# Performance work log

Hardware: AMD Instinct MI355X
Metric: run time of the kernel (lower is better)

The kernel has to match this reference:

```python
import jax, jax.numpy as jnp
import numpy as np

D = 512      # model dim
H = 8        # heads
HD = D // H  # head dim = 64
NQ = 2048    # n_query
NC = 4096    # n_context
EPS = 1e-5   # LayerNorm eps (torch default)


def setup_inputs() -> dict:
    key = jax.random.key(0)
    ks = jax.random.split(key, 12)
    s = 0.02
    return {
        "query_repr": jax.random.normal(ks[0], (NQ, D), dtype=jnp.float32),
        "context_repr": jax.random.normal(ks[1], (NC, D), dtype=jnp.float32),
        "query_coords": jax.random.uniform(ks[2], (NQ, 2), dtype=jnp.float32) * 10.0,
        "context_coords": jax.random.uniform(ks[3], (NC, 2), dtype=jnp.float32) * 10.0,
        "Wq": jax.random.normal(ks[4], (D, D), dtype=jnp.float32) * s,
        "bq": jnp.zeros((D,), jnp.float32),
        "Wk": jax.random.normal(ks[5], (D, D), dtype=jnp.float32) * s,
        "bk": jnp.zeros((D,), jnp.float32),
        "Wv": jax.random.normal(ks[6], (D, D), dtype=jnp.float32) * s,
        "bv": jnp.zeros((D,), jnp.float32),
        "Wo": jax.random.normal(ks[7], (D, D), dtype=jnp.float32) * s,
        "bo": jnp.zeros((D,), jnp.float32),
        "ln_g": jnp.ones((D,), jnp.float32),
        "ln_b": jnp.zeros((D,), jnp.float32),
        "log_scale": jnp.array(0.0, jnp.float32),          # log_distance_scale
        "bias_per_head": jnp.ones((H,), jnp.float32),      # distance_bias_per_head
    }


def reference(query_repr, context_repr, query_coords, context_coords,
              Wq, bq, Wk, bk, Wv, bv, Wo, bo, ln_g, ln_b,
              log_scale, bias_per_head):
    # pairwise Euclidean distances (NQ, NC)
    diff = query_coords[:, None, :] - context_coords[None, :, :]
    dist = jnp.sqrt(jnp.sum(diff * diff, axis=-1))
    # per-head additive attention bias (H, NQ, NC)
    bias = (-jnp.exp(log_scale) * dist)[None, :, :] * bias_per_head[:, None, None]

    # multi-head attention (batch=1, eval mode so dropout is identity)
    q = (query_repr @ Wq.T + bq).reshape(NQ, H, HD).transpose(1, 0, 2)    # (H, NQ, HD)
    k = (context_repr @ Wk.T + bk).reshape(NC, H, HD).transpose(1, 0, 2)  # (H, NC, HD)
    v = (context_repr @ Wv.T + bv).reshape(NC, H, HD).transpose(1, 0, 2)  # (H, NC, HD)

    scale = 1.0 / jnp.sqrt(jnp.float32(HD))
    scores = jnp.einsum('hqd,hkd->hqk', q, k) * scale + bias              # (H, NQ, NC)
    attn = jax.nn.softmax(scores, axis=-1)
    ctx = jnp.einsum('hqk,hkd->hqd', attn, v)                             # (H, NQ, HD)
    attended = ctx.transpose(1, 0, 2).reshape(NQ, D) @ Wo.T + bo          # (NQ, D)

    # residual + LayerNorm
    x = attended + query_repr
    mu = jnp.mean(x, axis=-1, keepdims=True)
    var = jnp.mean((x - mu) ** 2, axis=-1, keepdims=True)
    return (x - mu) / jnp.sqrt(var + EPS) * ln_g + ln_b
```

## Files before the change

kernel.cpp:

```cpp
#include <hip/hip_runtime.h>

#define D 512
#define H 8
#define HD 64
#define NQ 2048
#define NC 4096
#define SPLIT 8
#define CLEN (NC / SPLIT)
#define NT (CLEN / 32)
#define M0 3.0f
#define KP2 136
#define VP 40

typedef __attribute__((ext_vector_type(8))) short short8;
typedef __attribute__((ext_vector_type(4))) short short4v;
typedef __attribute__((ext_vector_type(4))) float float4v;
typedef __attribute__((ext_vector_type(4))) int int4v;

__device__ inline float bf2f(short s) {
    unsigned int u = ((unsigned int)(unsigned short)s) << 16;
    return __builtin_bit_cast(float, u);
}
__device__ inline short f2bf(float f) {
    unsigned int u = __builtin_bit_cast(unsigned int, f);
    u = (u + 0x7FFF + ((u >> 16) & 1)) >> 16;
    return (short)u;
}
__device__ inline int cvtpk(float a, float b) {
    int w;
    asm("v_cvt_pk_bf16_f32 %0, %1, %2" : "=v"(w) : "v"(a), "v"(b));
    return w;
}

__global__ __launch_bounds__(256) void cast_all(
    const float* __restrict__ s0, const float* __restrict__ s1,
    const float* __restrict__ s2, const float* __restrict__ s3,
    const float* __restrict__ s4, const float* __restrict__ s5,
    short* __restrict__ dst)
{
    int i = blockIdx.x * 256 + threadIdx.x;
    const float* src; int off;
    if      (i < 262144) { src = s0; off = i; }
    else if (i < 786432) { src = s1; off = i - 262144; }
    else if (i < 851968) { src = s2; off = i - 786432; }
    else if (i < 917504) { src = s3; off = i - 851968; }
    else if (i < 983040) { src = s4; off = i - 917504; }
    else                 { src = s5; off = i - 983040; }
    float4v v = ((const float4v*)src)[off];
    short4v o;
    o.x = f2bf(v.x); o.y = f2bf(v.y); o.z = f2bf(v.z); o.w = f2bf(v.w);
    ((short4v*)dst)[i] = o;
}

__global__ __launch_bounds__(256) void gemm_bt_bias(
    const short* __restrict__ X, const short* __restrict__ W,
    const float* __restrict__ bias, short* __restrict__ out, int M)
{
    int wave = threadIdx.x >> 6, lane = threadIdx.x & 63;
    int gt = blockIdx.x * 4 + wave;
    int tm = gt >> 3;
    int tg = gt & 7;
    if (tm >= (M >> 4)) return;
    int l15 = lane & 15, quad = lane >> 4;
    const short* xp = X + (tm * 16 + l15) * D + quad * 8;
    const short* wp = W + (tg * 64 + l15) * D + quad * 8;
    float4v a0 = {0,0,0,0}, a1 = {0,0,0,0}, a2 = {0,0,0,0}, a3 = {0,0,0,0};
#pragma unroll
    for (int k = 0; k < D; k += 32) {
        short8 a  = *(const short8*)(xp + k);
        short8 b0 = *(const short8*)(wp + k);
        short8 b1 = *(const short8*)(wp + 16 * D + k);
        short8 b2 = *(const short8*)(wp + 32 * D + k);
        short8 b3 = *(const short8*)(wp + 48 * D + k);
        a0 = __builtin_amdgcn_mfma_f32_16x16x32_bf16(a, b0, a0, 0, 0, 0);
        a1 = __builtin_amdgcn_mfma_f32_16x16x32_bf16(a, b1, a1, 0, 0, 0);
        a2 = __builtin_amdgcn_mfma_f32_16x16x32_bf16(a, b2, a2, 0, 0, 0);
        a3 = __builtin_amdgcn_mfma_f32_16x16x32_bf16(a, b3, a3, 0, 0, 0);
    }
    int orow = tm * 16 + quad * 4;
    float4v accs[4] = {a0, a1, a2, a3};
#pragma unroll
    for (int j = 0; j < 4; j++) {
        int col = tg * 64 + j * 16 + l15;
        float bv = bias[col];
#pragma unroll
        for (int r = 0; r < 4; r++)
            out[(orow + r) * D + col] = f2bf(accs[j][r] + bv);
    }
}

__global__ __launch_bounds__(256) void gemm_qkv(
    const short* __restrict__ Xq, const short* __restrict__ Xc,
    const short* __restrict__ Wq, const short* __restrict__ Wk,
    const short* __restrict__ Wv,
    const float* __restrict__ bq, const float* __restrict__ bk,
    const float* __restrict__ bv,
    short* __restrict__ Qout, short* __restrict__ Kout,
    short* __restrict__ VoutT)
{
    int wave = threadIdx.x >> 6, lane = threadIdx.x & 63;
    int l15 = lane & 15, quad = lane >> 4;
    int blk = blockIdx.x;
    if (blk < 256) {
        int gt = blk * 4 + wave;
        int tm = gt >> 3, tg = gt & 7;
        const short* xp = Xq + (tm * 16 + l15) * D + quad * 8;
        const short* wp = Wq + (tg * 64 + l15) * D + quad * 8;
        float4v a0 = {0,0,0,0}, a1 = {0,0,0,0}, a2 = {0,0,0,0}, a3 = {0,0,0,0};
#pragma unroll
        for (int k = 0; k < D; k += 32) {
            short8 a  = *(const short8*)(xp + k);
            short8 b0 = *(const short8*)(wp + k);
            short8 b1 = *(const short8*)(wp + 16 * D + k);
            short8 b2 = *(const short8*)(wp + 32 * D + k);
            short8 b3 = *(const short8*)(wp + 48 * D + k);
            a0 = __builtin_amdgcn_mfma_f32_16x16x32_bf16(a, b0, a0, 0, 0, 0);
            a1 = __builtin_amdgcn_mfma_f32_16x16x32_bf16(a, b1, a1, 0, 0, 0);
            a2 = __builtin_amdgcn_mfma_f32_16x16x32_bf16(a, b2, a2, 0, 0, 0);
            a3 = __builtin_amdgcn_mfma_f32_16x16x32_bf16(a, b3, a3, 0, 0, 0);
        }
        int orow = tm * 16 + quad * 4;
        float4v accs[4] = {a0, a1, a2, a3};
#pragma unroll
        for (int j = 0; j < 4; j++) {
            int col = tg * 64 + j * 16 + l15;
            float bb = bq[col];
#pragma unroll
            for (int r = 0; r < 4; r++)
                Qout[(orow + r) * D + col] = f2bf(accs[j][r] + bb);
        }
    } else {
        int gt = (blk - 256) * 4 + wave;
        int tm = gt >> 3, tg = gt & 7;
        const short* xp  = Xc + (tm * 16 + l15) * D + quad * 8;
        const short* wkp = Wk + (tg * 64 + l15) * D + quad * 8;
        const short* wvp = Wv + (tg * 64 + l15) * D + quad * 8;
        float4v k0 = {0,0,0,0}, k1 = {0,0,0,0}, k2 = {0,0,0,0}, k3 = {0,0,0,0};
        float4v v0 = {0,0,0,0}, v1 = {0,0,0,0}, v2 = {0,0,0,0}, v3 = {0,0,0,0};
#pragma unroll
        for (int k = 0; k < D; k += 32) {
            short8 a   = *(const short8*)(xp + k);
            short8 bk0 = *(const short8*)(wkp + k);
            short8 bk1 = *(const short8*)(wkp + 16 * D + k);
            short8 bk2 = *(const short8*)(wkp + 32 * D + k);
            short8 bk3 = *(const short8*)(wkp + 48 * D + k);
            short8 bv0 = *(const short8*)(wvp + k);
            short8 bv1 = *(const short8*)(wvp + 16 * D + k);
            short8 bv2 = *(const short8*)(wvp + 32 * D + k);
            short8 bv3 = *(const short8*)(wvp + 48 * D + k);
            k0 = __builtin_amdgcn_mfma_f32_16x16x32_bf16(a, bk0, k0, 0, 0, 0);
            k1 = __builtin_amdgcn_mfma_f32_16x16x32_bf16(a, bk1, k1, 0, 0, 0);
            k2 = __builtin_amdgcn_mfma_f32_16x16x32_bf16(a, bk2, k2, 0, 0, 0);
            k3 = __builtin_amdgcn_mfma_f32_16x16x32_bf16(a, bk3, k3, 0, 0, 0);
            v0 = __builtin_amdgcn_mfma_f32_16x16x32_bf16(a, bv0, v0, 0, 0, 0);
            v1 = __builtin_amdgcn_mfma_f32_16x16x32_bf16(a, bv1, v1, 0, 0, 0);
            v2 = __builtin_amdgcn_mfma_f32_16x16x32_bf16(a, bv2, v2, 0, 0, 0);
            v3 = __builtin_amdgcn_mfma_f32_16x16x32_bf16(a, bv3, v3, 0, 0, 0);
        }
        int orow = tm * 16 + quad * 4;
        {
            float4v accs[4] = {k0, k1, k2, k3};
#pragma unroll
            for (int j = 0; j < 4; j++) {
                int col = tg * 64 + j * 16 + l15;
                float bb = bk[col];
#pragma unroll
                for (int r = 0; r < 4; r++)
                    Kout[(orow + r) * D + col] = f2bf(accs[j][r] + bb);
            }
        }
        {
            int a = (orow & 31) >> 2;
            int posb = (a < 4) ? (8 * a) : (8 * (a - 4) + 4);
            int cp = (orow & ~31) + posb;
            float4v accs[4] = {v0, v1, v2, v3};
#pragma unroll
            for (int j = 0; j < 4; j++) {
                int col = tg * 64 + j * 16 + l15;
                float bb = bv[col];
                short4v o;
#pragma unroll
                for (int r = 0; r < 4; r++) o[r] = f2bf(accs[j][r] + bb);
                *(short4v*)(VoutT + (size_t)col * NC + cp) = o;
            }
        }
    }
}

__global__ __launch_bounds__(256) void gemm_res_ln(
    const short* __restrict__ X, const short* __restrict__ W,
    const float* __restrict__ bias, const float* __restrict__ resid,
    const float* __restrict__ g, const float* __restrict__ b,
    float* __restrict__ out)
{
    __shared__ float redS[4][4][4];
    __shared__ float redV[4][4][4];

    int wave = threadIdx.x >> 6, lane = threadIdx.x & 63;
    int l15 = lane & 15, quad = lane >> 4;
    int tm = blockIdx.x;
    const short* xp  = X + (tm * 16 + l15) * D + quad * 8;
    const short* wp0 = W + ((2 * wave) * 64 + l15) * D + quad * 8;
    const short* wp1 = wp0 + 64 * D;
    float4v a00 = {0,0,0,0}, a01 = {0,0,0,0}, a02 = {0,0,0,0}, a03 = {0,0,0,0};
    float4v a10 = {0,0,0,0}, a11 = {0,0,0,0}, a12 = {0,0,0,0}, a13 = {0,0,0,0};
#pragma unroll
    for (int k = 0; k < D; k += 32) {
        short8 a   = *(const short8*)(xp + k);
        short8 b00 = *(const short8*)(wp0 + k);
        short8 b01 = *(const short8*)(wp0 + 16 * D + k);
        short8 b02 = *(const short8*)(wp0 + 32 * D + k);
        short8 b03 = *(const short8*)(wp0 + 48 * D + k);
        short8 b10 = *(const short8*)(wp1 + k);
        short8 b11 = *(const short8*)(wp1 + 16 * D + k);
        short8 b12 = *(const short8*)(wp1 + 32 * D + k);
        short8 b13 = *(const short8*)(wp1 + 48 * D + k);
        a00 = __builtin_amdgcn_mfma_f32_16x16x32_bf16(a, b00, a00, 0, 0, 0);
        a01 = __builtin_amdgcn_mfma_f32_16x16x32_bf16(a, b01, a01, 0, 0, 0);
        a02 = __builtin_amdgcn_mfma_f32_16x16x32_bf16(a, b02, a02, 0, 0, 0);
        a03 = __builtin_amdgcn_mfma_f32_16x16x32_bf16(a, b03, a03, 0, 0, 0);
        a10 = __builtin_amdgcn_mfma_f32_16x16x32_bf16(a, b10, a10, 0, 0, 0);
        a11 = __builtin_amdgcn_mfma_f32_16x16x32_bf16(a, b11, a11, 0, 0, 0);
        a12 = __builtin_amdgcn_mfma_f32_16x16x32_bf16(a, b12, a12, 0, 0, 0);
        a13 = __builtin_amdgcn_mfma_f32_16x16x32_bf16(a, b13, a13, 0, 0, 0);
    }
    int orow = tm * 16 + quad * 4;
    float v[2][4][4];
    float4v accs[2][4] = {{a00, a01, a02, a03}, {a10, a11, a12, a13}};
#pragma unroll
    for (int t = 0; t < 2; t++) {
#pragma unroll
        for (int j = 0; j < 4; j++) {
            int col = (2 * wave + t) * 64 + j * 16 + l15;
            float bv = bias[col];
#pragma unroll
            for (int r = 0; r < 4; r++)
                v[t][j][r] = accs[t][j][r] + bv + resid[(orow + r) * D + col];
        }
    }
    float ps[4];
#pragma unroll
    for (int r = 0; r < 4; r++) {
        float s = 0.f;
#pragma unroll
        for (int t = 0; t < 2; t++)
#pragma unroll
            for (int j = 0; j < 4; j++) s += v[t][j][r];
#pragma unroll
        for (int off = 1; off < 16; off <<= 1) s += __shfl_xor(s, off);
        ps[r] = s;
    }
    if (l15 == 0) {
#pragma unroll
        for (int r = 0; r < 4; r++) redS[wave][quad][r] = ps[r];
    }
    __syncthreads();
    float mu[4];
#pragma unroll
    for (int r = 0; r < 4; r++)
        mu[r] = (redS[0][quad][r] + redS[1][quad][r] +
                 redS[2][quad][r] + redS[3][quad][r]) * (1.f / D);
#pragma unroll
    for (int r = 0; r < 4; r++) {
        float s = 0.f;
#pragma unroll
        for (int t = 0; t < 2; t++)
#pragma unroll
            for (int j = 0; j < 4; j++) {
                float d = v[t][j][r] - mu[r];
                s += d * d;
            }
#pragma unroll
        for (int off = 1; off < 16; off <<= 1) s += __shfl_xor(s, off);
        ps[r] = s;
    }
    if (l15 == 0) {
#pragma unroll
        for (int r = 0; r < 4; r++) redV[wave][quad][r] = ps[r];
    }
    __syncthreads();
    float rstd[4];
#pragma unroll
    for (int r = 0; r < 4; r++) {
        float var = (redV[0][quad][r] + redV[1][quad][r] +
                     redV[2][quad][r] + redV[3][quad][r]) * (1.f / D);
        rstd[r] = rsqrtf(var + 1e-5f);
    }
#pragma unroll
    for (int t = 0; t < 2; t++) {
#pragma unroll
        for (int j = 0; j < 4; j++) {
            int col = (2 * wave + t) * 64 + j * 16 + l15;
            float gc = g[col], bc = b[col];
#pragma unroll
            for (int r = 0; r < 4; r++)
                out[(orow + r) * D + col] =
                    (v[t][j][r] - mu[r]) * rstd[r] * gc + bc;
        }
    }
}

__global__ __launch_bounds__(256) void gemm_bt_bias_res_f32(
    const short* __restrict__ X, const short* __restrict__ W,
    const float* __restrict__ bias, const float* __restrict__ resid,
    float* __restrict__ out, int M)
{
    int wave = threadIdx.x >> 6, lane = threadIdx.x & 63;
    int gt = blockIdx.x * 4 + wave;
    int tm = gt >> 3;
    int tg = gt & 7;
    if (tm >= (M >> 4)) return;
    int l15 = lane & 15, quad = lane >> 4;
    const short* xp = X + (tm * 16 + l15) * D + quad * 8;
    const short* wp = W + (tg * 64 + l15) * D + quad * 8;
    float4v a0 = {0,0,0,0}, a1 = {0,0,0,0}, a2 = {0,0,0,0}, a3 = {0,0,0,0};
#pragma unroll
    for (int k = 0; k < D; k += 32) {
        short8 a  = *(const short8*)(xp + k);
        short8 b0 = *(const short8*)(wp + k);
        short8 b1 = *(const short8*)(wp + 16 * D + k);
        short8 b2 = *(const short8*)(wp + 32 * D + k);
        short8 b3 = *(const short8*)(wp + 48 * D + k);
        a0 = __builtin_amdgcn_mfma_f32_16x16x32_bf16(a, b0, a0, 0, 0, 0);
        a1 = __builtin_amdgcn_mfma_f32_16x16x32_bf16(a, b1, a1, 0, 0, 0);
        a2 = __builtin_amdgcn_mfma_f32_16x16x32_bf16(a, b2, a2, 0, 0, 0);
        a3 = __builtin_amdgcn_mfma_f32_16x16x32_bf16(a, b3, a3, 0, 0, 0);
    }
    int orow = tm * 16 + quad * 4;
    float4v accs[4] = {a0, a1, a2, a3};
#pragma unroll
    for (int j = 0; j < 4; j++) {
        int col = tg * 64 + j * 16 + l15;
        float bv = bias[col];
#pragma unroll
        for (int r = 0; r < 4; r++) {
            int q = orow + r;
            out[q * D + col] = accs[j][r] + bv + resid[q * D + col];
        }
    }
}

__global__ __launch_bounds__(256) void attn_mfma_split9(
    const short* __restrict__ Q, const short* __restrict__ K,
    const short* __restrict__ Vp,
    const float* __restrict__ qc, const float* __restrict__ cc,
    const float* __restrict__ log_scale, const float* __restrict__ bph,
    short* __restrict__ Opart, float* __restrict__ Lpart)
{
    __shared__ __align__(16) short Klds[2][32 * KP2];
    __shared__ __align__(16) short Vlds[2][128 * VP];
    __shared__ __align__(16) float ccl[512];

    int tid = threadIdx.x;
    int wave = tid >> 6, lane = tid & 63;
    int h0 = blockIdx.y * 2;
    int sp = blockIdx.z;
    int q0 = blockIdx.x * 64 + wave * 16;
    int quad = lane >> 4, l15 = lane & 15;
    int cbase = sp * CLEN;

    const float LOG2E = 1.4426950408889634f;
    const float escale = 0.125f * LOG2E;
    const float M0L = M0 * LOG2E;
    float ebase = __expf(log_scale[0]);
    float bh0 = ebase * bph[h0] * LOG2E;
    float bh1 = ebase * bph[h0 + 1] * LOG2E;

    const short* qp = Q + (q0 + l15) * D + h0 * HD + quad * 8;
    short8 qa0_0 = *(const short8*)(qp);
    short8 qa1_0 = *(const short8*)(qp + 32);
    short8 qa0_1 = *(const short8*)(qp + 64);
    short8 qa1_1 = *(const short8*)(qp + 96);

    float qx = qc[(q0 + l15) * 2];
    float qy = qc[(q0 + l15) * 2 + 1];

    float lacc0 = 0.f, lacc1 = 0.f;
    float4v O00 = {0,0,0,0}, O01 = {0,0,0,0}, O02 = {0,0,0,0}, O03 = {0,0,0,0};
    float4v O10 = {0,0,0,0}, O11 = {0,0,0,0}, O12 = {0,0,0,0}, O13 = {0,0,0,0};

    int kr_ = tid >> 3, kc_ = tid & 7;
    int vr_ = tid >> 2, vc_ = tid & 3;
    const short* kg  = K + (size_t)h0 * HD + kc_ * 8;
    const short* vg0 = Vp + (size_t)(h0 * HD + vr_) * NC + vc_ * 8;
    const short* vg1 = Vp + (size_t)(h0 * HD + 64 + vr_) * NC + vc_ * 8;
    short* kw0a = &Klds[0][kr_ * KP2 + kc_ * 8];
    short* kw1a = &Klds[1][kr_ * KP2 + kc_ * 8];
    short* vw0a = &Vlds[0][vr_ * VP + vc_ * 8];
    short* vw0b = &Vlds[0][(64 + vr_) * VP + vc_ * 8];
    short* vw1a = &Vlds[1][vr_ * VP + vc_ * 8];
    short* vw1b = &Vlds[1][(64 + vr_) * VP + vc_ * 8];

    short8 rka, rkb, rva, rvb;

#define LOADR(c0_)                                                             \
    {                                                                          \
        const short* kp_ = kg + (size_t)((c0_) + kr_) * D;                     \
        rka = *(const short8*)(kp_);                                           \
        rkb = *(const short8*)(kp_ + 64);                                      \
        rva = *(const short8*)(vg0 + (c0_));                                   \
        rvb = *(const short8*)(vg1 + (c0_));                                   \
    }

#define DSW0 { *(short8*)kw0a = rka; *(short8*)(kw0a + 64) = rkb;              \
               *(short8*)vw0a = rva; *(short8*)vw0b = rvb; }
#define DSW1 { *(short8*)kw1a = rka; *(short8*)(kw1a + 64) = rkb;              \
               *(short8*)vw1a = rva; *(short8*)vw1b = rvb; }

    const float2* ccp = (const float2*)ccl;

#define HEAD(hoff, QA0, QA1, BH, LACC, OA, OB, OC, OD)                         \
    {                                                                          \
        short8 k00 = *(const short8*)(kb + l15 * KP2 + (hoff) + quad * 8);     \
        short8 k01 = *(const short8*)(kb + l15 * KP2 + (hoff) + 32 + quad * 8);\
        short8 k10 = *(const short8*)(kb + (16 + l15) * KP2 + (hoff) + quad * 8);\
        short8 k11 = *(const short8*)(kb + (16 + l15) * KP2 + (hoff) + 32 + quad * 8);\
        float4v s0 = {0,0,0,0}, s1 = {0,0,0,0};                                \
        s0 = __builtin_amdgcn_mfma_f32_16x16x32_bf16(k00, QA0, s0, 0, 0, 0);   \
        s0 = __builtin_amdgcn_mfma_f32_16x16x32_bf16(k01, QA1, s0, 0, 0, 0);   \
        s1 = __builtin_amdgcn_mfma_f32_16x16x32_bf16(k10, QA0, s1, 0, 0, 0);   \
        s1 = __builtin_amdgcn_mfma_f32_16x16x32_bf16(k11, QA1, s1, 0, 0, 0);   \
        short8 v0 = *(const short8*)(vb + ((hoff) / 64 * 64 + l15) * VP + quad * 8);       \
        short8 v1 = *(const short8*)(vb + ((hoff) / 64 * 64 + 16 + l15) * VP + quad * 8);  \
        short8 v2 = *(const short8*)(vb + ((hoff) / 64 * 64 + 32 + l15) * VP + quad * 8);  \
        short8 v3 = *(const short8*)(vb + ((hoff) / 64 * 64 + 48 + l15) * VP + quad * 8);  \
        float p00 = exp2f(__fmaf_rn(s0[0], escale, __fmaf_rn(-(BH), dA0, -M0L)));\
        float p01 = exp2f(__fmaf_rn(s0[1], escale, __fmaf_rn(-(BH), dA1, -M0L)));\
        float p02 = exp2f(__fmaf_rn(s0[2], escale, __fmaf_rn(-(BH), dA2, -M0L)));\
        float p03 = exp2f(__fmaf_rn(s0[3], escale, __fmaf_rn(-(BH), dA3, -M0L)));\
        float p10 = exp2f(__fmaf_rn(s1[0], escale, __fmaf_rn(-(BH), dB0, -M0L)));\
        float p11 = exp2f(__fmaf_rn(s1[1], escale, __fmaf_rn(-(BH), dB1, -M0L)));\
        float p12 = exp2f(__fmaf_rn(s1[2], escale, __fmaf_rn(-(BH), dB2, -M0L)));\
        float p13 = exp2f(__fmaf_rn(s1[3], escale, __fmaf_rn(-(BH), dB3, -M0L)));\
        LACC += ((p00 + p01) + (p02 + p03)) + ((p10 + p11) + (p12 + p13));     \
        int4v pw;                                                              \
        pw.x = cvtpk(p00, p01); pw.y = cvtpk(p02, p03);                        \
        pw.z = cvtpk(p10, p11); pw.w = cvtpk(p12, p13);                        \
        short8 pa = __builtin_bit_cast(short8, pw);                            \
        OA = __builtin_amdgcn_mfma_f32_16x16x32_bf16(pa, v0, OA, 0, 0, 0);     \
        OB = __builtin_amdgcn_mfma_f32_16x16x32_bf16(pa, v1, OB, 0, 0, 0);     \
        OC = __builtin_amdgcn_mfma_f32_16x16x32_bf16(pa, v2, OC, 0, 0, 0);     \
        OD = __builtin_amdgcn_mfma_f32_16x16x32_bf16(pa, v3, OD, 0, 0, 0);     \
    }

#define COMPUTE_TILE(B, lo)                                                    \
    {                                                                          \
        const short* kb = &Klds[B][0];                                         \
        const short* vb = &Vlds[B][0];                                         \
        float2 ca0 = ccp[(lo) + 4 * quad + 0], cb0 = ccp[(lo) + 16 + 4 * quad + 0];\
        float2 ca1 = ccp[(lo) + 4 * quad + 1], cb1 = ccp[(lo) + 16 + 4 * quad + 1];\
        float2 ca2 = ccp[(lo) + 4 * quad + 2], cb2 = ccp[(lo) + 16 + 4 * quad + 2];\
        float2 ca3 = ccp[(lo) + 4 * quad + 3], cb3 = ccp[(lo) + 16 + 4 * quad + 3];\
        float dx, dy;                                                          \
        dx = qx - ca0.x; dy = qy - ca0.y;                                      \
        float dA0 = __builtin_amdgcn_sqrtf(__fmaf_rn(dx, dx, dy * dy));        \
        dx = qx - ca1.x; dy = qy - ca1.y;                                      \
        float dA1 = __builtin_amdgcn_sqrtf(__fmaf_rn(dx, dx, dy * dy));        \
        dx = qx - ca2.x; dy = qy - ca2.y;                                      \
        float dA2 = __builtin_amdgcn_sqrtf(__fmaf_rn(dx, dx, dy * dy));        \
        dx = qx - ca3.x; dy = qy - ca3.y;                                      \
        float dA3 = __builtin_amdgcn_sqrtf(__fmaf_rn(dx, dx, dy * dy));        \
        dx = qx - cb0.x; dy = qy - cb0.y;                                      \
        float dB0 = __builtin_amdgcn_sqrtf(__fmaf_rn(dx, dx, dy * dy));        \
        dx = qx - cb1.x; dy = qy - cb1.y;                                      \
        float dB1 = __builtin_amdgcn_sqrtf(__fmaf_rn(dx, dx, dy * dy));        \
        dx = qx - cb2.x; dy = qy - cb2.y;                                      \
        float dB2 = __builtin_amdgcn_sqrtf(__fmaf_rn(dx, dx, dy * dy));        \
        dx = qx - cb3.x; dy = qy - cb3.y;                                      \
        float dB3 = __builtin_amdgcn_sqrtf(__fmaf_rn(dx, dx, dy * dy));        \
        HEAD(0,  qa0_0, qa1_0, bh0, lacc0, O00, O01, O02, O03)                 \
        HEAD(64, qa0_1, qa1_1, bh1, lacc1, O10, O11, O12, O13)                 \
    }

    ((float2*)ccl)[tid] = ((const float2*)cc)[cbase + tid];
    LOADR(cbase);
    DSW0;
    LOADR(cbase + 32);
    __syncthreads();

    for (int t = 0; t < NT - 2; t += 2) {
        int c0 = cbase + t * 32;
        if (t == 8) {
            ((float2*)ccl)[tid] = ((const float2*)cc)[cbase + 256 + tid];
            __syncthreads();
        }
        DSW1;
        LOADR(c0 + 64);
        COMPUTE_TILE(0, (t & 7) * 32);
        __syncthreads();
        DSW0;
        LOADR(c0 + 96);
        COMPUTE_TILE(1, (t & 7) * 32 + 32);
        __syncthreads();
    }
    DSW1;
    COMPUTE_TILE(0, 192);
    __syncthreads();
    COMPUTE_TILE(1, 224);

#undef LOADR
#undef DSW0
#undef DSW1
#undef HEAD
#undef COMPUTE_TILE

    lacc0 += __shfl_xor(lacc0, 16);
    lacc0 += __shfl_xor(lacc0, 32);
    lacc1 += __shfl_xor(lacc1, 16);
    lacc1 += __shfl_xor(lacc1, 32);

    long base0 = (long)(sp * H + h0) * NQ;
    long base1 = base0 + NQ;
    float4v Oarr0[4] = {O00, O01, O02, O03};
    float4v Oarr1[4] = {O10, O11, O12, O13};
#pragma unroll
    for (int t = 0; t < 4; t++) {
#pragma unroll
        for (int r = 0; r < 4; r++) {
            int q = q0 + quad * 4 + r;
            Opart[(base0 + q) * HD + t * 16 + l15] = f2bf(Oarr0[t][r]);
            Opart[(base1 + q) * HD + t * 16 + l15] = f2bf(Oarr1[t][r]);
        }
    }
    if (lane < 16) {
        Lpart[base0 + q0 + lane] = lacc0;
        Lpart[base1 + q0 + lane] = lacc1;
    }
}

__global__ __launch_bounds__(256) void attn_combine(
    const short* __restrict__ Opart, const float* __restrict__ Lpart,
    short* __restrict__ Att)
{
    int id = blockIdx.x * 256 + threadIdx.x;
    int d = id & 63;
    int q = (id >> 6) & (NQ - 1);
    int h = id >> 17;
    float L = 0.f, acc = 0.f;
#pragma unroll
    for (int s = 0; s < SPLIT; s++) {
        long b = (long)(s * H + h) * NQ + q;
        L   += Lpart[b];
        acc += bf2f(Opart[b * HD + d]);
    }
    Att[q * D + h * HD + d] = f2bf(acc / L);
}

__global__ __launch_bounds__(256) void attn_mfma(
    const short* __restrict__ Q, const short* __restrict__ K,
    const short* __restrict__ V,
    const float* __restrict__ qc, const float* __restrict__ cc,
    const float* __restrict__ log_scale, const float* __restrict__ bph,
    short* __restrict__ out)
{
    __shared__ short Vt[HD][48];
    __shared__ short P[4][16][48];
    int wave = threadIdx.x >> 6, lane = threadIdx.x & 63;
    int h = blockIdx.y;
    int q0 = blockIdx.x * 64 + wave * 16;
    int quad = lane >> 4, l15 = lane & 15;
    const float scale = 0.125f;
    float bh = __expf(log_scale[0]) * bph[h];
    const short* qp = Q + (q0 + l15) * D + h * HD + quad * 8;
    short8 qa0 = *(const short8*)(qp);
    short8 qa1 = *(const short8*)(qp + 32);
    float qx[4], qy[4];
#pragma unroll
    for (int r = 0; r < 4; r++) {
        int q = q0 + quad * 4 + r;
        qx[r] = qc[q * 2]; qy[r] = qc[q * 2 + 1];
    }
    float m[4], l[4];
    float4v O[4];
#pragma unroll
    for (int r = 0; r < 4; r++) { m[r] = -1e30f; l[r] = 0.f; }
#pragma unroll
    for (int t = 0; t < 4; t++) O[t] = (float4v){0.f, 0.f, 0.f, 0.f};
    for (int c0 = 0; c0 < NC; c0 += 32) {
        __syncthreads();
        {
            int c = threadIdx.x >> 3;
            int dblk = (threadIdx.x & 7) * 8;
            short8 vv = *(const short8*)(V + (c0 + c) * D + h * HD + dblk);
#pragma unroll
            for (int j = 0; j < 8; j++) Vt[dblk + j][c] = vv[j];
        }
        const short* kp0 = K + (c0 + l15) * D + h * HD + quad * 8;
        const short* kp1 = kp0 + 16 * D;
        short8 kb00 = *(const short8*)(kp0);
        short8 kb01 = *(const short8*)(kp0 + 32);
        short8 kb10 = *(const short8*)(kp1);
        short8 kb11 = *(const short8*)(kp1 + 32);
        float4v s0 = {0,0,0,0}, s1 = {0,0,0,0};
        s0 = __builtin_amdgcn_mfma_f32_16x16x32_bf16(qa0, kb00, s0, 0, 0, 0);
        s0 = __builtin_amdgcn_mfma_f32_16x16x32_bf16(qa1, kb01, s0, 0, 0, 0);
        s1 = __builtin_amdgcn_mfma_f32_16x16x32_bf16(qa0, kb10, s1, 0, 0, 0);
        s1 = __builtin_amdgcn_mfma_f32_16x16x32_bf16(qa1, kb11, s1, 0, 0, 0);
        int cA = c0 + l15, cB = cA + 16;
        float cxA = cc[cA * 2], cyA = cc[cA * 2 + 1];
        float cxB = cc[cB * 2], cyB = cc[cB * 2 + 1];
#pragma unroll
        for (int r = 0; r < 4; r++) {
            float dxA = qx[r] - cxA, dyA = qy[r] - cyA;
            float dxB = qx[r] - cxB, dyB = qy[r] - cyB;
            float v0 = s0[r] * scale - bh * sqrtf(dxA * dxA + dyA * dyA);
            float v1 = s1[r] * scale - bh * sqrtf(dxB * dxB + dyB * dyB);
            float mx = fmaxf(v0, v1);
#pragma unroll
            for (int off = 1; off < 16; off <<= 1) mx = fmaxf(mx, __shfl_xor(mx, off));
            float mnew = fmaxf(m[r], mx);
            float alpha = __expf(m[r] - mnew);
            float p0 = __expf(v0 - mnew);
            float p1 = __expf(v1 - mnew);
            float ps = p0 + p1;
#pragma unroll
            for (int off = 1; off < 16; off <<= 1) ps += __shfl_xor(ps, off);
            l[r] = l[r] * alpha + ps;
            m[r] = mnew;
#pragma unroll
            for (int t = 0; t < 4; t++) O[t][r] *= alpha;
            P[wave][quad * 4 + r][l15]      = f2bf(p0);
            P[wave][quad * 4 + r][16 + l15] = f2bf(p1);
        }
        __syncthreads();
        short8 pa = *(const short8*)(&P[wave][l15][quad * 8]);
#pragma unroll
        for (int t = 0; t < 4; t++) {
            short8 vb = *(const short8*)(&Vt[t * 16 + l15][quad * 8]);
            O[t] = __builtin_amdgcn_mfma_f32_16x16x32_bf16(pa, vb, O[t], 0, 0, 0);
        }
    }
#pragma unroll
    for (int t = 0; t < 4; t++) {
#pragma unroll
        for (int r = 0; r < 4; r++) {
            int q = q0 + quad * 4 + r;
            out[q * D + h * HD + t * 16 + l15] = f2bf(O[t][r] / l[r]);
        }
    }
}

__global__ __launch_bounds__(256) void layernorm_kernel(
    const float* __restrict__ X, const float* __restrict__ g,
    const float* __restrict__ b, float* __restrict__ out)
{
    int wave = threadIdx.x >> 6, lane = threadIdx.x & 63;
    int row = blockIdx.x * 4 + wave;
    const float* xp = X + row * D;
    float v[8];
    float s = 0.f;
#pragma unroll
    for (int i = 0; i < 8; i++) { v[i] = xp[lane + i * 64]; s += v[i]; }
#pragma unroll
    for (int off = 1; off < 64; off <<= 1) s += __shfl_xor(s, off);
    float mu = s * (1.f / D);
    float var = 0.f;
#pragma unroll
    for (int i = 0; i < 8; i++) { float d = v[i] - mu; var += d * d; }
#pragma unroll
    for (int off = 1; off < 64; off <<= 1) var += __shfl_xor(var, off);
    float rstd = rsqrtf(var * (1.f / D) + 1e-5f);
#pragma unroll
    for (int i = 0; i < 8; i++) {
        int c = lane + i * 64;
        out[row * D + c] = (v[i] - mu) * rstd * g[c] + b[c];
    }
}

extern "C" void kernel_launch(void* const* d_in, const int* in_sizes, int n_in,
                              void* d_out, int out_size, void* d_ws, size_t ws_size,
                              hipStream_t stream) {
    const float* query_repr     = (const float*)d_in[0];
    const float* context_repr   = (const float*)d_in[1];
    const float* query_coords   = (const float*)d_in[2];
    const float* context_coords = (const float*)d_in[3];
    const float* Wq = (const float*)d_in[4];
    const float* bq = (const float*)d_in[5];
    const float* Wk = (const float*)d_in[6];
    const float* bk = (const float*)d_in[7];
    const float* Wv = (const float*)d_in[8];
    const float* bv = (const float*)d_in[9];
    const float* Wo = (const float*)d_in[10];
    const float* bo = (const float*)d_in[11];
    const float* ln_g = (const float*)d_in[12];
    const float* ln_b = (const float*)d_in[13];
    const float* log_scale = (const float*)d_in[14];
    const float* bph = (const float*)d_in[15];

    short* ws = (short*)d_ws;
    short* Xq_bf = ws;
    short* Xc_bf = Xq_bf + NQ * D;
    short* Wq_bf = Xc_bf + NC * D;
    short* Wk_bf = Wq_bf + D * D;
    short* Wv_bf = Wk_bf + D * D;
    short* Wo_bf = Wv_bf + D * D;
    short* Qw  = Wo_bf + D * D;
    short* Kw  = Qw + NQ * D;
    short* Vw  = Kw + NC * D;
    short* Att = Vw + NC * D;
    float* Xf  = (float*)(Att + NQ * D);
    short* Opart = (short*)(Xf + NQ * D);
    float* Lpart = (float*)(Opart + (size_t)SPLIT * H * NQ * HD);
    size_t ws_needed_split = ((char*)(Lpart + (size_t)SPLIT * H * NQ)) - (char*)d_ws;

    cast_all<<<dim3(4096), 256, 0, stream>>>(
        query_repr, context_repr, Wq, Wk, Wv, Wo, Xq_bf);

    if (ws_size >= ws_needed_split) {
        gemm_qkv<<<dim3(768), 256, 0, stream>>>(
            Xq_bf, Xc_bf, Wq_bf, Wk_bf, Wv_bf, bq, bk, bv, Qw, Kw, Vw);
        attn_mfma_split9<<<dim3(NQ / 64, H / 2, SPLIT), 256, 0, stream>>>(
            Qw, Kw, Vw, query_coords, context_coords, log_scale, bph,
            Opart, Lpart);
        attn_combine<<<dim3(H * NQ * HD / 256), 256, 0, stream>>>(
            Opart, Lpart, Att);
        gemm_res_ln<<<dim3(NQ / 16), 256, 0, stream>>>(
            Att, Wo_bf, bo, query_repr, ln_g, ln_b, (float*)d_out);
    } else {
        gemm_bt_bias<<<dim3((NQ / 16) * 8 / 4), 256, 0, stream>>>(
            Xq_bf, Wq_bf, bq, Qw, NQ);
        gemm_bt_bias<<<dim3((NC / 16) * 8 / 4), 256, 0, stream>>>(
            Xc_bf, Wk_bf, bk, Kw, NC);
        gemm_bt_bias<<<dim3((NC / 16) * 8 / 4), 256, 0, stream>>>(
            Xc_bf, Wv_bf, bv, Vw, NC);
        attn_mfma<<<dim3(NQ / 64, H), 256, 0, stream>>>(
            Qw, Kw, Vw, query_coords, context_coords, log_scale, bph, Att);
        gemm_bt_bias_res_f32<<<dim3((NQ / 16) * 8 / 4), 256, 0, stream>>>(
            Att, Wo_bf, bo, query_repr, Xf, NQ);
        layernorm_kernel<<<dim3(NQ / 4), 256, 0, stream>>>(
            Xf, ln_g, ln_b, (float*)d_out);
    }
}
```

Baseline: 202.6 us.

## Rewrite QKV projection as LDS-tiled double-buffered MFMA GEMM

Replaces the per-wave QKV projection, which streamed A and B fragments straight from global memory, with a block-tiled GEMM. Each block computes a 128x64 tile with 32-wide K slices staged through padded, double-buffered shared memory, and the next slice's global load overlaps the current MFMAs. This increases operand reuse and cuts redundant global and L2 traffic. In exchange it gives up the shared A load that K and V used to get from one fused pass, and adds barriers and LDS traffic.

```diff
diff --git a/kernel.cpp b/kernel.cpp
--- a/kernel.cpp
+++ b/kernel.cpp
@@ -11,6 +11,11 @@
 #define M0 3.0f
 #define KP2 136
 #define VP 40
+
+#define TBM 128
+#define TBN 64
+#define TBK 32
+#define TPAD 40
 
 typedef __attribute__((ext_vector_type(8))) short short8;
 typedef __attribute__((ext_vector_type(4))) short short4v;
@@ -89,7 +94,7 @@
     }
 }
 
-__global__ __launch_bounds__(256) void gemm_qkv(
+__global__ __launch_bounds__(256) void gemm_qkv_tiled(
     const short* __restrict__ Xq, const short* __restrict__ Xc,
     const short* __restrict__ Wq, const short* __restrict__ Wk,
     const short* __restrict__ Wv,
@@ -98,90 +103,128 @@
     short* __restrict__ Qout, short* __restrict__ Kout,
     short* __restrict__ VoutT)
 {
-    int wave = threadIdx.x >> 6, lane = threadIdx.x & 63;
-    int l15 = lane & 15, quad = lane >> 4;
+    __shared__ __align__(16) short Ab[2][TBM * TPAD];
+    __shared__ __align__(16) short Bb[2][TBN * TPAD];
+
+    int tid = threadIdx.x;
+    int wave = tid >> 6, lane = tid & 63;
+    int quad = lane >> 4, l15 = lane & 15;
+
     int blk = blockIdx.x;
-    if (blk < 256) {
-        int gt = blk * 4 + wave;
-        int tm = gt >> 3, tg = gt & 7;
-        const short* xp = Xq + (tm * 16 + l15) * D + quad * 8;
-        const short* wp = Wq + (tg * 64 + l15) * D + quad * 8;
-        float4v a0 = {0,0,0,0}, a1 = {0,0,0,0}, a2 = {0,0,0,0}, a3 = {0,0,0,0};
-#pragma unroll
-        for (int k = 0; k < D; k += 32) {
-            short8 a  = *(const short8*)(xp + k);
-            short8 b0 = *(const short8*)(wp + k);
-            short8 b1 = *(const short8*)(wp + 16 * D + k);
-            short8 b2 = *(const short8*)(wp + 32 * D + k);
-            short8 b3 = *(const short8*)(wp + 48 * D + k);
-            a0 = __builtin_amdgcn_mfma_f32_16x16x32_bf16(a, b0, a0, 0, 0, 0);
-            a1 = __builtin_amdgcn_mfma_f32_16x16x32_bf16(a, b1, a1, 0, 0, 0);
-            a2 = __builtin_amdgcn_mfma_f32_16x16x32_bf16(a, b2, a2, 0, 0, 0);
-            a3 = __builtin_amdgcn_mfma_f32_16x16x32_bf16(a, b3, a3, 0, 0, 0);
-        }
-        int orow = tm * 16 + quad * 4;
-        float4v accs[4] = {a0, a1, a2, a3};
-#pragma unroll
-        for (int j = 0; j < 4; j++) {
-            int col = tg * 64 + j * 16 + l15;
-            float bb = bq[col];
-#pragma unroll
-            for (int r = 0; r < 4; r++)
-                Qout[(orow + r) * D + col] = f2bf(accs[j][r] + bb);
-        }
+    const short *X, *W;
+    const float* bias;
+    short* outp;
+    int bm, bn, vmode;
+    if (blk < 128) {
+        X = Xq; W = Wq; bias = bq; outp = Qout; vmode = 0;
+        bm = (blk >> 3) * TBM; bn = (blk & 7) * TBN;
+    } else if (blk < 384) {
+        int b = blk - 128;
+        X = Xc; W = Wk; bias = bk; outp = Kout; vmode = 0;
+        bm = (b >> 3) * TBM; bn = (b & 7) * TBN;
     } else {
-        int gt = (blk - 256) * 4 + wave;
-        int tm = gt >> 3, tg = gt & 7;
-        const short* xp  = Xc + (tm * 16 + l15) * D + quad * 8;
-        const short* wkp = Wk + (tg * 64 + l15) * D + quad * 8;
-        const short* wvp = Wv + (tg * 64 + l15) * D + quad * 8;
-        float4v k0 = {0,0,0,0}, k1 = {0,0,0,0}, k2 = {0,0,0,0}, k3 = {0,0,0,0};
-        float4v v0 = {0,0,0,0}, v1 = {0,0,0,0}, v2 = {0,0,0,0}, v3 = {0,0,0,0};
-#pragma unroll
-        for (int k = 0; k < D; k += 32) {
-            short8 a   = *(const short8*)(xp + k);
-            short8 bk0 = *(const short8*)(wkp + k);
-            short8 bk1 = *(const short8*)(wkp + 16 * D + k);
-            short8 bk2 = *(const short8*)(wkp + 32 * D + k);
-            short8 bk3 = *(const short8*)(wkp + 48 * D + k);
-            short8 bv0 = *(const short8*)(wvp + k);
-            short8 bv1 = *(const short8*)(wvp + 16 * D + k);
-            short8 bv2 = *(const short8*)(wvp + 32 * D + k);
-            short8 bv3 = *(const short8*)(wvp + 48 * D + k);
-            k0 = __builtin_amdgcn_mfma_f32_16x16x32_bf16(a, bk0, k0, 0, 0, 0);
-            k1 = __builtin_amdgcn_mfma_f32_16x16x32_bf16(a, bk1, k1, 0, 0, 0);
-            k2 = __builtin_amdgcn_mfma_f32_16x16x32_bf16(a, bk2, k2, 0, 0, 0);
-            k3 = __builtin_amdgcn_mfma_f32_16x16x32_bf16(a, bk3, k3, 0, 0, 0);
-            v0 = __builtin_amdgcn_mfma_f32_16x16x32_bf16(a, bv0, v0, 0, 0, 0);
-            v1 = __builtin_amdgcn_mfma_f32_16x16x32_bf16(a, bv1, v1, 0, 0, 0);
-            v2 = __builtin_amdgcn_mfma_f32_16x16x32_bf16(a, bv2, v2, 0, 0, 0);
-            v3 = __builtin_amdgcn_mfma_f32_16x16x32_bf16(a, bv3, v3, 0, 0, 0);
-        }
-        int orow = tm * 16 + quad * 4;
-        {
-            float4v accs[4] = {k0, k1, k2, k3};
-#pragma unroll
-            for (int j = 0; j < 4; j++) {
-                int col = tg * 64 + j * 16 + l15;
-                float bb = bk[col];
+        int b = blk - 384;
+        X = Xc; W = Wv; bias = bv; outp = VoutT; vmode = 1;
+        bm = (b >> 3) * TBM; bn = (b & 7) * TBN;
+    }
+
+    int ar = tid >> 1, ac = (tid & 1) * 16;
+    int br = tid >> 2, bc = (tid & 3) * 8;
+    const short* ag = X + (size_t)(bm + ar) * D + ac;
+    const short* bg = W + (size_t)(bn + br) * D + bc;
+    short* aw0 = &Ab[0][ar * TPAD + ac];
+    short* aw1 = &Ab[1][ar * TPAD + ac];
+    short* bw0 = &Bb[0][br * TPAD + bc];
+    short* bw1 = &Bb[1][br * TPAD + bc];
+
+    short8 ra0, ra1, rb;
+
+#define GLOAD(ks) { const short* ap_ = ag + (ks) * TBK;                        \
+        ra0 = *(const short8*)(ap_);                                           \
+        ra1 = *(const short8*)(ap_ + 8);                                       \
+        rb  = *(const short8*)(bg + (ks) * TBK); }
+#define GDSW0 { *(short8*)aw0 = ra0; *(short8*)(aw0 + 8) = ra1;                \
+                *(short8*)bw0 = rb; }
+#define GDSW1 { *(short8*)aw1 = ra0; *(short8*)(aw1 + 8) = ra1;                \
+                *(short8*)bw1 = rb; }
+
+    float4v c00 = {0,0,0,0}, c01 = {0,0,0,0}, c02 = {0,0,0,0}, c03 = {0,0,0,0};
+    float4v c10 = {0,0,0,0}, c11 = {0,0,0,0}, c12 = {0,0,0,0}, c13 = {0,0,0,0};
+
+#define GCOMP(B)                                                               \
+    {                                                                          \
+        const short* abase = &Ab[B][(wave * 32 + l15) * TPAD + quad * 8];      \
+        const short* bbase = &Bb[B][l15 * TPAD + quad * 8];                    \
+        short8 a0 = *(const short8*)(abase);                                   \
+        short8 a1 = *(const short8*)(abase + 16 * TPAD);                       \
+        short8 b0 = *(const short8*)(bbase);                                   \
+        short8 b1 = *(const short8*)(bbase + 16 * TPAD);                       \
+        short8 b2 = *(const short8*)(bbase + 32 * TPAD);                       \
+        short8 b3 = *(const short8*)(bbase + 48 * TPAD);                       \
+        c00 = __builtin_amdgcn_mfma_f32_16x16x32_bf16(a0, b0, c00, 0, 0, 0);   \
+        c01 = __builtin_amdgcn_mfma_f32_16x16x32_bf16(a0, b1, c01, 0, 0, 0);   \
+        c02 = __builtin_amdgcn_mfma_f32_16x16x32_bf16(a0, b2, c02, 0, 0, 0);   \
+        c03 = __builtin_amdgcn_mfma_f32_16x16x32_bf16(a0, b3, c03, 0, 0, 0);   \
+        c10 = __builtin_amdgcn_mfma_f32_16x16x32_bf16(a1, b0, c10, 0, 0, 0);   \
+        c11 = __builtin_amdgcn_mfma_f32_16x16x32_bf16(a1, b1, c11, 0, 0, 0);   \
+        c12 = __builtin_amdgcn_mfma_f32_16x16x32_bf16(a1, b2, c12, 0, 0, 0);   \
+        c13 = __builtin_amdgcn_mfma_f32_16x16x32_bf16(a1, b3, c13, 0, 0, 0);   \
+    }
+
+    GLOAD(0);
+    GDSW0;
+    GLOAD(1);
+    __syncthreads();
+
+    for (int t = 0; t < 14; t += 2) {
+        GDSW1;
+        GLOAD(t + 2);
+        GCOMP(0);
+        __syncthreads();
+        GDSW0;
+        GLOAD(t + 3);
+        GCOMP(1);
+        __syncthreads();
+    }
+    GDSW1;
+    GCOMP(0);
+    __syncthreads();
+    GCOMP(1);
+
+#undef GLOAD
+#undef GDSW0
+#undef GDSW1
+#undef GCOMP
+
+    float4v accs[2][4] = {{c00, c01, c02, c03}, {c10, c11, c12, c13}};
+    if (vmode == 0) {
+#pragma unroll
+        for (int mf = 0; mf < 2; mf++) {
+            int orow = bm + wave * 32 + mf * 16 + quad * 4;
+#pragma unroll
+            for (int nf = 0; nf < 4; nf++) {
+                int col = bn + nf * 16 + l15;
+                float bb_ = bias[col];
 #pragma unroll
                 for (int r = 0; r < 4; r++)
-                    Kout[(orow + r) * D + col] = f2bf(accs[j][r] + bb);
+                    outp[(size_t)(orow + r) * D + col] = f2bf(accs[mf][nf][r] + bb_);
             }
         }
-        {
+    } else {
+#pragma unroll
+        for (int mf = 0; mf < 2; mf++) {
+            int orow = bm + wave * 32 + mf * 16 + quad * 4;
             int a = (orow & 31) >> 2;
             int posb = (a < 4) ? (8 * a) : (8 * (a - 4) + 4);
             int cp = (orow & ~31) + posb;
-            float4v accs[4] = {v0, v1, v2, v3};
-#pragma unroll
-            for (int j = 0; j < 4; j++) {
-                int col = tg * 64 + j * 16 + l15;
-                float bb = bv[col];
+#pragma unroll
+            for (int nf = 0; nf < 4; nf++) {
+                int col = bn + nf * 16 + l15;
+                float bb_ = bias[col];
                 short4v o;
 #pragma unroll
-                for (int r = 0; r < 4; r++) o[r] = f2bf(accs[j][r] + bb);
-                *(short4v*)(VoutT + (size_t)col * NC + cp) = o;
+                for (int r = 0; r < 4; r++) o[r] = f2bf(accs[mf][nf][r] + bb_);
+                *(short4v*)(outp + (size_t)col * NC + cp) = o;
             }
         }
     }
@@ -707,7 +750,7 @@
         query_repr, context_repr, Wq, Wk, Wv, Wo, Xq_bf);
 
     if (ws_size >= ws_needed_split) {
-        gemm_qkv<<<dim3(768), 256, 0, stream>>>(
+        gemm_qkv_tiled<<<dim3(640), 256, 0, stream>>>(
             Xq_bf, Xc_bf, Wq_bf, Wk_bf, Wv_bf, bq, bk, bv, Qw, Kw, Vw);
         attn_mfma_split9<<<dim3(NQ / 64, H / 2, SPLIT), 256, 0, stream>>>(
             Qw, Kw, Vw, query_coords, context_coords, log_scale, bph,
```

After: 173.7 us. 1.17x faster.
